# Performance work log

Hardware: AMD Instinct MI355X
Metric: run time of the kernel (lower is better)

Reference implementation:

```python
import jax, jax.numpy as jnp
import numpy as np

B, N, D_MODEL, H, DK, DV = 8, 512, 512, 8, 64, 64
MAX_DIST = 512
NUM_REL = 2 * MAX_DIST - 1  # 1023


def setup_inputs() -> dict:
    key = jax.random.key(0)
    ks = jax.random.split(key, 12)
    s = 0.02
    return {
        "X": jax.random.normal(ks[0], (B, N, D_MODEL), jnp.float32),
        "Wq": jax.random.normal(ks[1], (D_MODEL, H * DK), jnp.float32) * s,
        "bq": jnp.zeros((H * DK,), jnp.float32),
        "Wk": jax.random.normal(ks[2], (D_MODEL, H * DK), jnp.float32) * s,
        "bk": jnp.zeros((H * DK,), jnp.float32),
        "Wv": jax.random.normal(ks[3], (D_MODEL, H * DV), jnp.float32) * s,
        "bv": jnp.zeros((H * DV,), jnp.float32),
        "Wo": jax.random.normal(ks[4], (H * DV, D_MODEL), jnp.float32) * s,
        "bo": jnp.zeros((D_MODEL,), jnp.float32),
        "P_k": jax.random.normal(ks[5], (NUM_REL, H), jnp.float32),
        "P_v": jax.random.normal(ks[6], (NUM_REL, H, DV), jnp.float32),
    }


def reference(X, Wq, bq, Wk, bk, Wv, bv, Wo, bo, P_k, P_v):
    b, n, d = X.shape
    scale = 1.0 / jnp.sqrt(jnp.float32(DK))
    # projections -> [b, h, n, d]
    Q = (X @ Wq + bq).reshape(b, n, H, DK).transpose(0, 2, 1, 3)
    K = (X @ Wk + bk).reshape(b, n, H, DK).transpose(0, 2, 1, 3)
    V = (X @ Wv + bv).reshape(b, n, H, DV).transpose(0, 2, 1, 3)
    # relative index: rel[i, j] = zero_offset + (j - i)
    zero_offset = NUM_REL // 2
    rel = zero_offset + (jnp.arange(n)[None, :] - jnp.arange(n)[:, None])  # [n, n]
    A_k = P_k[rel]  # [n, n, h]
    scores = (jnp.einsum("bhid,bhjd->bhij", Q, K) + A_k.transpose(2, 0, 1)[None]) * scale
    attn = jax.nn.softmax(scores, axis=-1)  # [b, h, n, n]
    # standard value mixing + relative value mixing (einsum avoids the
    # explicit [b,h,n,n,dv] broadcast the torch code materializes; same math)
    A_v = P_v[rel]  # [n, n, h, dv]
    out = jnp.einsum("bhij,bhjd->bhid", attn, V) + jnp.einsum("bhij,ijhd->bhid", attn, A_v)
    out = out.transpose(0, 2, 1, 3).reshape(b, n, H * DV)
    return out @ Wo + bo
```

## Files before the change

### kernel.cpp

```cpp
#include <hip/hip_runtime.h>
#include <math.h>

#define Bc 8
#define Nseq 512
#define DM 512
#define Hh 8
#define NUMREL 1023
#define ZOFF 511
#define STR 552

typedef short bf16x8 __attribute__((ext_vector_type(8)));
typedef float f32x4 __attribute__((ext_vector_type(4)));

__device__ __forceinline__ unsigned short f2bf(float f) {
  unsigned u = __builtin_bit_cast(unsigned, f);
  u += 0x7fff + ((u >> 16) & 1);
  return (unsigned short)(u >> 16);
}
__device__ __forceinline__ float bf2f(unsigned short h) {
  unsigned u = ((unsigned)h) << 16;
  return __builtin_bit_cast(float, u);
}

typedef __attribute__((address_space(3))) unsigned int as3_uint;
typedef __attribute__((address_space(1))) const unsigned int as1_uint;
__device__ __forceinline__ void gl_lds16(const void* g, void* l) {
  __builtin_amdgcn_global_load_lds((as1_uint*)g, (as3_uint*)l, 16, 0, 0);
}

__global__ __launch_bounds__(256) void prep_all(
    const float* __restrict__ X, const float* __restrict__ Wq,
    const float* __restrict__ Wk, const float* __restrict__ Wv,
    const float* __restrict__ Wo, const float* __restrict__ Pk,
    const float* __restrict__ Pv,
    unsigned short* __restrict__ XbF, unsigned short* __restrict__ WqF,
    unsigned short* __restrict__ WkF, unsigned short* __restrict__ WvF,
    unsigned short* __restrict__ WoFh, unsigned short* __restrict__ WoFl,
    float* __restrict__ Pkt, unsigned short* __restrict__ PvF2) {
  __shared__ float tbuf[5120];
  const int bid = blockIdx.x;
  const int tid = threadIdx.x;

  if (bid < 1024) {
    const int w = tid >> 6, lane = tid & 63;
    const int r = bid * 4 + w;
    const float* src = X + (size_t)r * DM + lane * 8;
    float4 a = *(const float4*)src;
    float4 b = *(const float4*)(src + 4);
    ushort4 o0, o1;
    o0.x = f2bf(a.x); o0.y = f2bf(a.y); o0.z = f2bf(a.z); o0.w = f2bf(a.w);
    o1.x = f2bf(b.x); o1.y = f2bf(b.y); o1.z = f2bf(b.z); o1.w = f2bf(b.w);
    const int mc = r >> 4, kf = lane >> 2, l = (lane & 3) * 16 + (r & 15);
    size_t flat = (((size_t)mc * 16 + kf) * 64 + l) * 8;
    *(ushort4*)(XbF + flat) = o0;
    *(ushort4*)(XbF + flat + 4) = o1;
  } else if (bid < 2304) {
    const int idx = bid - 1024;
    const int z = idx >> 8, r256 = idx & 255;
    const int bx = r256 & 15, by = r256 >> 4;
    const float* src = z == 0 ? Wq : z == 1 ? Wk : z == 2 ? Wv : Wo;
    unsigned short* dst = z == 0 ? WqF : z == 1 ? WkF : z == 2 ? WvF : z == 3 ? WoFh : WoFl;
    const int k0 = by * 32, n0 = bx * 32;
#pragma unroll
    for (int u = 0; u < 4; ++u) {
      int i2 = u * 256 + tid, r = i2 >> 5, c = i2 & 31;
      tbuf[r * 33 + c] = src[(size_t)(k0 + r) * DM + n0 + c];
    }
    __syncthreads();
    const int ncl = tid >> 7, l = (tid >> 1) & 63, eh = tid & 1;
    const int nl = ncl * 16 + (l & 15);
    const int klb = (l >> 4) * 8 + eh * 4;
    ushort4 o;
    {
      float v0 = tbuf[(klb + 0) * 33 + nl], v1 = tbuf[(klb + 1) * 33 + nl];
      float v2 = tbuf[(klb + 2) * 33 + nl], v3 = tbuf[(klb + 3) * 33 + nl];
      unsigned short h0 = f2bf(v0), h1 = f2bf(v1), h2 = f2bf(v2), h3 = f2bf(v3);
      if (z == 4) {
        h0 = f2bf(v0 - bf2f(h0)); h1 = f2bf(v1 - bf2f(h1));
        h2 = f2bf(v2 - bf2f(h2)); h3 = f2bf(v3 - bf2f(h3));
      }
      o.x = h0; o.y = h1; o.z = h2; o.w = h3;
    }
    size_t flat = (((size_t)((n0 >> 4) + ncl) * 16 + (k0 >> 5)) * 64 + l) * 8 + eh * 4;
    *(ushort4*)(dst + flat) = o;
  } else if (bid < 2344) {
    const int idx = bid - 2304;
    const int gx = idx % 5, h = idx / 5;
    const int g = gx * 256 + tid;
    if (g < 1040)
      Pkt[(size_t)h * 1040 + g] = (g < NUMREL) ? Pk[(size_t)g * Hh + h] : 0.f;
  } else {
    const int idx = bid - 2344;
    const int gx = idx & 15, h = idx >> 4;
    const int g0 = gx * 64;
#pragma unroll
    for (int u = 0; u < 20; ++u) {
      int i2 = u * 256 + tid, r = i2 >> 6, c = i2 & 63;
      int g = g0 + r;
      tbuf[r * 64 + c] = (g < NUMREL) ? Pv[(size_t)g * 512 + h * 64 + c] : 0.f;
    }
    __syncthreads();
#pragma unroll
    for (int av = 0; av < 2; ++av)
#pragma unroll
      for (int gtl = 0; gtl < 2; ++gtl) {
        int gt = (g0 >> 5) + gtl;
#pragma unroll
        for (int dt = 0; dt < 4; ++dt) {
          size_t base = ((((size_t)av * Hh + h) * 4 + dt) * 32 + gt) * 512;
          int i2 = tid * 2;
          int l = i2 >> 3, e = i2 & 7;
          int gr = av * 16 + gtl * 32 + (l >> 4) * 8 + e;
          int dcol = dt * 16 + (l & 15);
          ushort2 o;
          o.x = f2bf(tbuf[gr * 64 + dcol]);
          o.y = f2bf(tbuf[(gr + 1) * 64 + dcol]);
          *(ushort2*)(PvF2 + base + i2) = o;
        }
      }
  }
}

__global__ __launch_bounds__(256, 2) void gemm_qkv(const unsigned short* __restrict__ XbF,
                                                   const unsigned short* __restrict__ WqF,
                                                   const unsigned short* __restrict__ WkF,
                                                   const unsigned short* __restrict__ WvF,
                                                   const float* __restrict__ bq,
                                                   const float* __restrict__ bk,
                                                   const float* __restrict__ bv,
                                                   unsigned short* __restrict__ Qb,
                                                   unsigned short* __restrict__ KF,
                                                   unsigned short* __restrict__ VF) {
  const int flat = blockIdx.x;
  const int xcd = flat & 7, g = flat >> 3;
  const int by = xcd * 8 + (g & 7), bx = g >> 3;
  const int bm = by * 64, bn = bx * 64;
  const int mc0 = bm >> 4, nc0 = bn >> 4;
  const int tid = threadIdx.x, w = tid >> 6, lane = tid & 63;
  const int lo = lane & 15, quad = lane >> 4;
  const int mh = (w >> 1) * 2, nh = (w & 1) * 2;

  __shared__ __align__(16) unsigned short stg[2][32 * 512];

  const unsigned short* srcArr = w == 0 ? XbF : w == 1 ? WqF : w == 2 ? WkF : WvF;
  const int rowbase = (w == 0) ? mc0 : nc0;

#define STAGE(buf, ks)                                                             \
  do {                                                                             \
    _Pragma("unroll") for (int t = 0; t < 8; ++t) {                                \
      gl_lds16(srcArr +                                                            \
                   (((size_t)(rowbase + (t >> 1)) * 16 + 2 * (ks) + (t & 1)) * 512) + \
                   lane * 8,                                                       \
               &stg[buf][(w * 8 + t) * 512]);                                      \
    }                                                                              \
  } while (0)

  f32x4 acc[3][2][2] = {};
  STAGE(0, 0);
  int cur = 0;
#pragma unroll
  for (int ks = 0; ks < 8; ++ks) {
    __syncthreads();
    if (ks < 7) STAGE(cur ^ 1, ks + 1);
#pragma unroll
    for (int kf = 0; kf < 2; ++kf) {
      bf16x8 af[2], bq_[2], bk_[2], bv_[2];
#pragma unroll
      for (int i = 0; i < 2; ++i)
        af[i] = *(const bf16x8*)(&stg[cur][((mh + i) * 2 + kf) * 512 + lane * 8]);
#pragma unroll
      for (int j = 0; j < 2; ++j) {
        bq_[j] = *(const bf16x8*)(&stg[cur][(8 + (nh + j) * 2 + kf) * 512 + lane * 8]);
        bk_[j] = *(const bf16x8*)(&stg[cur][(16 + (nh + j) * 2 + kf) * 512 + lane * 8]);
        bv_[j] = *(const bf16x8*)(&stg[cur][(24 + (nh + j) * 2 + kf) * 512 + lane * 8]);
      }
#pragma unroll
      for (int i = 0; i < 2; ++i)
#pragma unroll
        for (int j = 0; j < 2; ++j) {
          acc[0][i][j] = __builtin_amdgcn_mfma_f32_16x16x32_bf16(af[i], bq_[j], acc[0][i][j], 0, 0, 0);
          acc[1][i][j] = __builtin_amdgcn_mfma_f32_16x16x32_bf16(af[i], bk_[j], acc[1][i][j], 0, 0, 0);
          acc[2][i][j] = __builtin_amdgcn_mfma_f32_16x16x32_bf16(af[i], bv_[j], acc[2][i][j], 0, 0, 0);
        }
    }
    cur ^= 1;
  }
#undef STAGE

  const int mt = (w >> 1) * 32, nt = (w & 1) * 32;
#pragma unroll
  for (int z = 0; z < 3; ++z) {
    const float* bias = z == 0 ? bq : z == 1 ? bk : bv;
#pragma unroll
    for (int i = 0; i < 2; ++i)
#pragma unroll
      for (int j = 0; j < 2; ++j) {
        int col = bn + nt + j * 16 + lo;
        int h = col >> 6, d = col & 63;
        float bb = bias[col];
#pragma unroll
        for (int r = 0; r < 4; ++r) {
          int row = bm + mt + i * 16 + quad * 4 + r;
          int b = row >> 9, is = row & 511;
          int bh = b * Hh + h;
          unsigned short val = f2bf(acc[z][i][j][r] + bb);
          if (z == 0) {
            Qb[((size_t)bh * Nseq + is) * 64 + d] = val;
          } else if (z == 1) {
            int jt = is >> 4, kf2 = d >> 5, l = ((d >> 3) & 3) * 16 + (is & 15), e = d & 7;
            KF[(((size_t)bh * 32 + jt) * 2 + kf2) * 512 + l * 8 + e] = val;
          } else {
            int dt = d >> 4, ks = is >> 5, l = ((is >> 3) & 3) * 16 + (d & 15), e = is & 7;
            VF[(((size_t)bh * 4 + dt) * 16 + ks) * 512 + l * 8 + e] = val;
          }
        }
      }
  }
}

__global__ __launch_bounds__(256, 3) void attn_fused(
    const unsigned short* __restrict__ Qb,
    const unsigned short* __restrict__ KF,
    const unsigned short* __restrict__ VF,
    const float* __restrict__ Pkt,
    const unsigned short* __restrict__ PvF2,
    unsigned short* __restrict__ AwFh,
    unsigned short* __restrict__ AwFl) {
  const int flat = blockIdx.x;
  const int h = flat & 7;
  const int grp = flat >> 3;
  const int b = grp >> 4;
  const int p = grp & 15;
  const int itA = (p >> 1) * 4 + (p & 1);
  const int i0A = itA * 16;
  const int bh = b * Hh + h;
  const int tid = threadIdx.x, w = tid >> 6, lane = tid & 63;
  const int lo = lane & 15, quad = lane >> 4;

  __shared__ __align__(16) unsigned short stg[2][4096];
  __shared__ __align__(16) unsigned short pstA[16 * STR];
  __shared__ __align__(16) unsigned short pstB[16 * STR];
  __shared__ float pk_lds[560];

  const int TB = 464 - i0A;

  int4 z4; z4.x = z4.y = z4.z = z4.w = 0;
  for (int c = tid; c < 16 * STR / 8; c += 256) {
    ((int4*)pstA)[c] = z4;
    ((int4*)pstB)[c] = z4;
  }
  for (int c = tid; c < 140; c += 256)
    *(float4*)(pk_lds + c * 4) = *(const float4*)(Pkt + (size_t)h * 1040 + TB + c * 4);

  const unsigned short* qA = Qb + ((size_t)bh * Nseq + i0A + lo) * 64;
  const unsigned short* qB = Qb + ((size_t)bh * Nseq + i0A + 32 + lo) * 64;
  bf16x8 qa0 = *(const bf16x8*)(qA + quad * 8);
  bf16x8 qa1 = *(const bf16x8*)(qA + 32 + quad * 8);
  bf16x8 qb0 = *(const bf16x8*)(qB + quad * 8);
  bf16x8 qb1 = *(const bf16x8*)(qB + 32 + quad * 8);

  const unsigned short* KFb = KF + (size_t)bh * 64 * 512;
  const unsigned short* VFb = VF + ((size_t)bh * 4 + w) * 16 * 512;
  const int aP = (TB >> 4) & 1, gtB = TB >> 5;
  const unsigned short* PFb = PvF2 + ((((size_t)aP * Hh + h) * 4 + w) * 32 + gtB) * 512;

#define KSTAGE(g, buf)                                                     \
  do {                                                                     \
    _Pragma("unroll") for (int c = 0; c < 2; ++c)                          \
        gl_lds16(KFb + ((size_t)(w * 8 + (g)) * 2 + c) * 512 + lane * 8,   \
                 &stg[buf][(w * 2 + c) * 512]);                            \
  } while (0)
#define VSTAGE(g, buf)                                                     \
  do {                                                                     \
    _Pragma("unroll") for (int c = 0; c < 2; ++c)                          \
        gl_lds16(VFb + ((size_t)(2 * (g) + c)) * 512 + lane * 8,           \
                 &stg[buf][(w * 2 + c) * 512]);                            \
  } while (0)
#define PSTAGE(g, buf)                                                     \
  do {                                                                     \
    _Pragma("unroll") for (int c = 0; c < 2; ++c)                          \
        gl_lds16(PFb + ((size_t)(2 * (g) + c)) * 512 + lane * 8,           \
                 &stg[buf][(w * 2 + c) * 512]);                            \
  } while (0)

  KSTAGE(0, 0);
  __syncthreads();

  float svA[8][4], svB[8][4];
  float mA[4] = {-1e30f, -1e30f, -1e30f, -1e30f};
  float mB[4] = {-1e30f, -1e30f, -1e30f, -1e30f};
#pragma unroll
  for (int g = 0; g < 8; ++g) {
    bf16x8 k0 = *(const bf16x8*)(&stg[g & 1][(w * 2 + 0) * 512 + lane * 8]);
    bf16x8 k1 = *(const bf16x8*)(&stg[g & 1][(w * 2 + 1) * 512 + lane * 8]);
    if (g < 7) KSTAGE(g + 1, (g + 1) & 1);
    f32x4 cA = {0.f, 0.f, 0.f, 0.f};
    f32x4 cB = {0.f, 0.f, 0.f, 0.f};
    cA = __builtin_amdgcn_mfma_f32_16x16x32_bf16(qa0, k0, cA, 0, 0, 0);
    cA = __builtin_amdgcn_mfma_f32_16x16x32_bf16(qa1, k1, cA, 0, 0, 0);
    cB = __builtin_amdgcn_mfma_f32_16x16x32_bf16(qb0, k0, cB, 0, 0, 0);
    cB = __builtin_amdgcn_mfma_f32_16x16x32_bf16(qb1, k1, cB, 0, 0, 0);
    int j = w * 128 + g * 16 + lo;
#pragma unroll
    for (int r = 0; r < 4; ++r) {
      int rl = quad * 4 + r;
      int idx = j - rl + 15;
      float vA = (cA[r] + pk_lds[idx + 32]) * 0.125f;
      float vB = (cB[r] + pk_lds[idx]) * 0.125f;
      svA[g][r] = vA; svB[g][r] = vB;
      mA[r] = fmaxf(mA[r], vA);
      mB[r] = fmaxf(mB[r], vB);
    }
    __syncthreads();
  }

  float* redm = (float*)&stg[1][0];
  float* redl = (float*)&stg[1][256];
#pragma unroll
  for (int m = 1; m <= 8; m <<= 1)
#pragma unroll
    for (int r = 0; r < 4; ++r) {
      mA[r] = fmaxf(mA[r], __shfl_xor(mA[r], m));
      mB[r] = fmaxf(mB[r], __shfl_xor(mB[r], m));
    }
  if (lo == 0)
#pragma unroll
    for (int r = 0; r < 4; ++r) {
      redm[(0 * 4 + w) * 16 + quad * 4 + r] = mA[r];
      redm[(1 * 4 + w) * 16 + quad * 4 + r] = mB[r];
    }
  __syncthreads();
  float mfA[4], mfB[4];
#pragma unroll
  for (int r = 0; r < 4; ++r) {
    int rl = quad * 4 + r;
    mfA[r] = fmaxf(fmaxf(redm[rl], redm[16 + rl]), fmaxf(redm[32 + rl], redm[48 + rl]));
    mfB[r] = fmaxf(fmaxf(redm[64 + rl], redm[80 + rl]), fmaxf(redm[96 + rl], redm[112 + rl]));
  }
  float lA[4] = {0.f, 0.f, 0.f, 0.f}, lB[4] = {0.f, 0.f, 0.f, 0.f};
#pragma unroll
  for (int s = 0; s < 8; ++s)
#pragma unroll
    for (int r = 0; r < 4; ++r) {
      float eA = __expf(svA[s][r] - mfA[r]);
      float eB = __expf(svB[s][r] - mfB[r]);
      svA[s][r] = eA; svB[s][r] = eB;
      lA[r] += eA; lB[r] += eB;
    }
#pragma unroll
  for (int m = 1; m <= 8; m <<= 1)
#pragma unroll
    for (int r = 0; r < 4; ++r) {
      lA[r] += __shfl_xor(lA[r], m);
      lB[r] += __shfl_xor(lB[r], m);
    }
  if (lo == 0)
#pragma unroll
    for (int r = 0; r < 4; ++r) {
      redl[(0 * 4 + w) * 16 + quad * 4 + r] = lA[r];
      redl[(1 * 4 + w) * 16 + quad * 4 + r] = lB[r];
    }
  __syncthreads();
#pragma unroll
  for (int r = 0; r < 4; ++r) {
    int rl = quad * 4 + r;
    float liA = 1.f / (redl[rl] + redl[16 + rl] + redl[32 + rl] + redl[48 + rl]);
    float liB = 1.f / (redl[64 + rl] + redl[80 + rl] + redl[96 + rl] + redl[112 + rl]);
#pragma unroll
    for (int s = 0; s < 8; ++s) {
      int j = w * 128 + s * 16 + lo;
      pstA[rl * STR + 16 + j] = f2bf(svA[s][r] * liA);
      pstB[rl * STR + 16 + j] = f2bf(svB[s][r] * liB);
    }
  }
  VSTAGE(0, 0);
  __syncthreads();

  f32x4 oA = {0.f, 0.f, 0.f, 0.f};
  f32x4 oB = {0.f, 0.f, 0.f, 0.f};
#pragma unroll
  for (int g = 0; g < 8; ++g) {
    bf16x8 v0 = *(const bf16x8*)(&stg[g & 1][(w * 2 + 0) * 512 + lane * 8]);
    bf16x8 v1 = *(const bf16x8*)(&stg[g & 1][(w * 2 + 1) * 512 + lane * 8]);
    if (g < 7) VSTAGE(g + 1, (g + 1) & 1);
    else PSTAGE(0, 0);
#pragma unroll
    for (int c = 0; c < 2; ++c) {
      int ks = 2 * g + c;
      bf16x8 vv = c ? v1 : v0;
      bf16x8 pA = *(const bf16x8*)(&pstA[lo * STR + 16 + ks * 32 + quad * 8]);
      bf16x8 pB = *(const bf16x8*)(&pstB[lo * STR + 16 + ks * 32 + quad * 8]);
      oA = __builtin_amdgcn_mfma_f32_16x16x32_bf16(pA, vv, oA, 0, 0, 0);
      oB = __builtin_amdgcn_mfma_f32_16x16x32_bf16(pB, vv, oB, 0, 0, 0);
    }
    __syncthreads();
  }

#pragma unroll
  for (int g = 0; g < 9; ++g) {
    bf16x8 p0 = *(const bf16x8*)(&stg[g & 1][(w * 2 + 0) * 512 + lane * 8]);
    bf16x8 p1 = *(const bf16x8*)(&stg[g & 1][(w * 2 + 1) * 512 + lane * 8]);
    if (g < 8) PSTAGE(g + 1, (g + 1) & 1);
#pragma unroll
    for (int c = 0; c < 2; ++c) {
      int cg = 2 * g + c;
      bf16x8 pvf = c ? p1 : p0;
      if (cg < 17) {
        union { bf16x8 v; unsigned short s8[8]; } pa;
        if (cg == 16 && quad >= 2) {
#pragma unroll
          for (int e = 0; e < 8; ++e) pa.s8[e] = 0;
        } else {
          int base = lo * STR + cg * 32 + quad * 8 + lo + 1;
#pragma unroll
          for (int e = 0; e < 8; ++e) pa.s8[e] = pstB[base + e];
        }
        oB = __builtin_amdgcn_mfma_f32_16x16x32_bf16(pa.v, pvf, oB, 0, 0, 0);
      }
      if (cg >= 1) {
        int ksA = cg - 1;
        union { bf16x8 v; unsigned short s8[8]; } pa;
        if (ksA == 16 && quad >= 2) {
#pragma unroll
          for (int e = 0; e < 8; ++e) pa.s8[e] = 0;
        } else {
          int base = lo * STR + ksA * 32 + quad * 8 + lo + 1;
#pragma unroll
          for (int e = 0; e < 8; ++e) pa.s8[e] = pstA[base + e];
        }
        oA = __builtin_amdgcn_mfma_f32_16x16x32_bf16(pa.v, pvf, oA, 0, 0, 0);
      }
    }
    __syncthreads();
  }

  const int kf = h * 2 + (w >> 1);
  const int lhi = ((w & 1) * 2 + (lo >> 3)) * 16;
#pragma unroll
  for (int t = 0; t < 2; ++t) {
    f32x4 o = t ? oB : oA;
    int mc = b * 32 + itA + t * 2;
#pragma unroll
    for (int r = 0; r < 4; ++r) {
      float ov = o[r];
      unsigned short hi = f2bf(ov);
      unsigned short lov = f2bf(ov - bf2f(hi));
      size_t fl = (((size_t)mc * 16 + kf) * 64 + lhi + quad * 4 + r) * 8 + (lo & 7);
      AwFh[fl] = hi;
      AwFl[fl] = lov;
    }
  }
#undef KSTAGE
#undef VSTAGE
#undef PSTAGE
}

__global__ __launch_bounds__(256, 2) void gemm_final(const unsigned short* __restrict__ AhF,
                                                     const unsigned short* __restrict__ AlF,
                                                     const unsigned short* __restrict__ BhF,
                                                     const unsigned short* __restrict__ BlF,
                                                     const float* __restrict__ bo,
                                                     float* __restrict__ out) {
  const int flat = blockIdx.x;
  const int xcd = flat & 7, g = flat >> 3;
  const int by = xcd * 8 + (g & 7), bx = g >> 3;
  const int bm = by * 64, bn = bx * 64;
  const int mc0 = bm >> 4, nc0 = bn >> 4;
  const int tid = threadIdx.x, w = tid >> 6, lane = tid & 63;
  const int lo = lane & 15, quad = lane >> 4;
  const int mh = (w >> 1) * 2, nh = (w & 1) * 2;

  __shared__ __align__(16) unsigned short stg[2][32 * 512];

  const unsigned short* srcArr = w == 0 ? AhF : w == 1 ? AlF : w == 2 ? BhF : BlF;
  const int rowbase = (w < 2) ? mc0 : nc0;

#define STAGE2(buf, ks)                                                            \
  do {                                                                             \
    _Pragma("unroll") for (int t = 0; t < 8; ++t) {                                \
      gl_lds16(srcArr +                                                            \
                   (((size_t)(rowbase + (t >> 1)) * 16 + 2 * (ks) + (t & 1)) * 512) + \
                   lane * 8,                                                       \
               &stg[buf][(w * 8 + t) * 512]);                                      \
    }                                                                              \
  } while (0)

  f32x4 acc[2][2] = {};
  STAGE2(0, 0);
  int cur = 0;
#pragma unroll
  for (int ks = 0; ks < 8; ++ks) {
    __syncthreads();
    if (ks < 7) STAGE2(cur ^ 1, ks + 1);
#pragma unroll
    for (int kf = 0; kf < 2; ++kf) {
      bf16x8 ah[2], al[2], bh[2], bl[2];
#pragma unroll
      for (int i = 0; i < 2; ++i) {
        ah[i] = *(const bf16x8*)(&stg[cur][((mh + i) * 2 + kf) * 512 + lane * 8]);
        al[i] = *(const bf16x8*)(&stg[cur][(8 + (mh + i) * 2 + kf) * 512 + lane * 8]);
      }
#pragma unroll
      for (int j = 0; j < 2; ++j) {
        bh[j] = *(const bf16x8*)(&stg[cur][(16 + (nh + j) * 2 + kf) * 512 + lane * 8]);
        bl[j] = *(const bf16x8*)(&stg[cur][(24 + (nh + j) * 2 + kf) * 512 + lane * 8]);
      }
#pragma unroll
      for (int i = 0; i < 2; ++i)
#pragma unroll
        for (int j = 0; j < 2; ++j) {
          acc[i][j] = __builtin_amdgcn_mfma_f32_16x16x32_bf16(ah[i], bh[j], acc[i][j], 0, 0, 0);
          acc[i][j] = __builtin_amdgcn_mfma_f32_16x16x32_bf16(ah[i], bl[j], acc[i][j], 0, 0, 0);
          acc[i][j] = __builtin_amdgcn_mfma_f32_16x16x32_bf16(al[i], bh[j], acc[i][j], 0, 0, 0);
        }
    }
    cur ^= 1;
  }
#undef STAGE2

  const int mt = (w >> 1) * 32, nt = (w & 1) * 32;
#pragma unroll
  for (int i = 0; i < 2; ++i)
#pragma unroll
    for (int j = 0; j < 2; ++j) {
      int col = bn + nt + j * 16 + lo;
      float bb = bo[col];
#pragma unroll
      for (int r = 0; r < 4; ++r) {
        int row = bm + mt + i * 16 + quad * 4 + r;
        out[(size_t)row * DM + col] = acc[i][j][r] + bb;
      }
    }
}

extern "C" void kernel_launch(void* const* d_in, const int* in_sizes, int n_in,
                              void* d_out, int out_size, void* d_ws, size_t ws_size,
                              hipStream_t stream) {
  const float* X  = (const float*)d_in[0];
  const float* Wq = (const float*)d_in[1];
  const float* bq = (const float*)d_in[2];
  const float* Wk = (const float*)d_in[3];
  const float* bk = (const float*)d_in[4];
  const float* Wv = (const float*)d_in[5];
  const float* bv = (const float*)d_in[6];
  const float* Wo = (const float*)d_in[7];
  const float* bo = (const float*)d_in[8];
  const float* Pk = (const float*)d_in[9];
  const float* Pv = (const float*)d_in[10];
  float* out = (float*)d_out;

  char* p = (char*)d_ws;
  const size_t szX    = (size_t)Bc * Nseq * DM * 2;
  const size_t szW    = (size_t)DM * DM * 2;
  const size_t szPkt  = (size_t)Hh * 1040 * 4;
  const size_t szPvF2 = (size_t)2 * Hh * 4 * 32 * 512 * 2;
  const size_t szQKV  = (size_t)Bc * Hh * Nseq * 64 * 2;
  unsigned short* XbF  = (unsigned short*)p; p += szX;
  unsigned short* WqF  = (unsigned short*)p; p += szW;
  unsigned short* WkF  = (unsigned short*)p; p += szW;
  unsigned short* WvF  = (unsigned short*)p; p += szW;
  unsigned short* WoFh = (unsigned short*)p; p += szW;
  unsigned short* WoFl = (unsigned short*)p; p += szW;
  float*          Pkt  = (float*)p;          p += (szPkt + 255) & ~(size_t)255;
  unsigned short* PvF2 = (unsigned short*)p; p += szPvF2;
  unsigned short* Qb   = (unsigned short*)p; p += szQKV;
  unsigned short* KF   = (unsigned short*)p; p += szQKV;
  unsigned short* VF   = (unsigned short*)p; p += szQKV;
  unsigned short* AwFh = (unsigned short*)p; p += szX;
  unsigned short* AwFl = (unsigned short*)p; p += szX;

  dim3 blk(256);
  prep_all<<<dim3(2472), blk, 0, stream>>>(X, Wq, Wk, Wv, Wo, Pk, Pv,
                                           XbF, WqF, WkF, WvF, WoFh, WoFl, Pkt, PvF2);
  gemm_qkv<<<dim3(512), blk, 0, stream>>>(XbF, WqF, WkF, WvF, bq, bk, bv, Qb, KF, VF);
  attn_fused<<<dim3(1024), blk, 0, stream>>>(Qb, KF, VF, Pkt, PvF2, AwFh, AwFl);
  gemm_final<<<dim3(512), blk, 0, stream>>>(AwFh, AwFl, WoFh, WoFl, bo, out);
}
```

Measured before the change: 147.2 us.

## Switch bf16 pipeline to fp16 and drop split-precision output projection

Replaces bf16 conversions and MFMA calls with fp16 throughout, relying on fp16's extra mantissa bits to drop the hi/lo split for Wo and the attention output. This removes one weight-prep slice, halves the staged data and cuts MFMA count threefold in the final GEMM. Softmax normalization is deferred: unnormalized exponentials are written to LDS as fp16 and scaled at the end, with the value and relative-position accumulators kept separate. Risks fp16 range overflow or precision loss on the unnormalized probabilities and weights.

```diff
diff --git a/kernel.cpp b/kernel.cpp
--- a/kernel.cpp
+++ b/kernel.cpp
@@ -9,17 +9,12 @@
 #define ZOFF 511
 #define STR 552
 
-typedef short bf16x8 __attribute__((ext_vector_type(8)));
+typedef _Float16 half8 __attribute__((ext_vector_type(8)));
 typedef float f32x4 __attribute__((ext_vector_type(4)));
 
-__device__ __forceinline__ unsigned short f2bf(float f) {
-  unsigned u = __builtin_bit_cast(unsigned, f);
-  u += 0x7fff + ((u >> 16) & 1);
-  return (unsigned short)(u >> 16);
-}
-__device__ __forceinline__ float bf2f(unsigned short h) {
-  unsigned u = ((unsigned)h) << 16;
-  return __builtin_bit_cast(float, u);
+__device__ __forceinline__ unsigned short f2h(float f) {
+  _Float16 h = (_Float16)f;
+  return __builtin_bit_cast(unsigned short, h);
 }
 
 typedef __attribute__((address_space(3))) unsigned int as3_uint;
@@ -35,7 +30,7 @@
     const float* __restrict__ Pv,
     unsigned short* __restrict__ XbF, unsigned short* __restrict__ WqF,
     unsigned short* __restrict__ WkF, unsigned short* __restrict__ WvF,
-    unsigned short* __restrict__ WoFh, unsigned short* __restrict__ WoFl,
+    unsigned short* __restrict__ WoF,
     float* __restrict__ Pkt, unsigned short* __restrict__ PvF2) {
   __shared__ float tbuf[5120];
   const int bid = blockIdx.x;
@@ -48,18 +43,18 @@
     float4 a = *(const float4*)src;
     float4 b = *(const float4*)(src + 4);
     ushort4 o0, o1;
-    o0.x = f2bf(a.x); o0.y = f2bf(a.y); o0.z = f2bf(a.z); o0.w = f2bf(a.w);
-    o1.x = f2bf(b.x); o1.y = f2bf(b.y); o1.z = f2bf(b.z); o1.w = f2bf(b.w);
+    o0.x = f2h(a.x); o0.y = f2h(a.y); o0.z = f2h(a.z); o0.w = f2h(a.w);
+    o1.x = f2h(b.x); o1.y = f2h(b.y); o1.z = f2h(b.z); o1.w = f2h(b.w);
     const int mc = r >> 4, kf = lane >> 2, l = (lane & 3) * 16 + (r & 15);
     size_t flat = (((size_t)mc * 16 + kf) * 64 + l) * 8;
     *(ushort4*)(XbF + flat) = o0;
     *(ushort4*)(XbF + flat + 4) = o1;
-  } else if (bid < 2304) {
+  } else if (bid < 2048) {
     const int idx = bid - 1024;
     const int z = idx >> 8, r256 = idx & 255;
     const int bx = r256 & 15, by = r256 >> 4;
     const float* src = z == 0 ? Wq : z == 1 ? Wk : z == 2 ? Wv : Wo;
-    unsigned short* dst = z == 0 ? WqF : z == 1 ? WkF : z == 2 ? WvF : z == 3 ? WoFh : WoFl;
+    unsigned short* dst = z == 0 ? WqF : z == 1 ? WkF : z == 2 ? WvF : WoF;
     const int k0 = by * 32, n0 = bx * 32;
 #pragma unroll
     for (int u = 0; u < 4; ++u) {
@@ -71,26 +66,20 @@
     const int nl = ncl * 16 + (l & 15);
     const int klb = (l >> 4) * 8 + eh * 4;
     ushort4 o;
-    {
-      float v0 = tbuf[(klb + 0) * 33 + nl], v1 = tbuf[(klb + 1) * 33 + nl];
-      float v2 = tbuf[(klb + 2) * 33 + nl], v3 = tbuf[(klb + 3) * 33 + nl];
-      unsigned short h0 = f2bf(v0), h1 = f2bf(v1), h2 = f2bf(v2), h3 = f2bf(v3);
-      if (z == 4) {
-        h0 = f2bf(v0 - bf2f(h0)); h1 = f2bf(v1 - bf2f(h1));
-        h2 = f2bf(v2 - bf2f(h2)); h3 = f2bf(v3 - bf2f(h3));
-      }
-      o.x = h0; o.y = h1; o.z = h2; o.w = h3;
-    }
+    o.x = f2h(tbuf[(klb + 0) * 33 + nl]);
+    o.y = f2h(tbuf[(klb + 1) * 33 + nl]);
+    o.z = f2h(tbuf[(klb + 2) * 33 + nl]);
+    o.w = f2h(tbuf[(klb + 3) * 33 + nl]);
     size_t flat = (((size_t)((n0 >> 4) + ncl) * 16 + (k0 >> 5)) * 64 + l) * 8 + eh * 4;
     *(ushort4*)(dst + flat) = o;
-  } else if (bid < 2344) {
-    const int idx = bid - 2304;
+  } else if (bid < 2088) {
+    const int idx = bid - 2048;
     const int gx = idx % 5, h = idx / 5;
     const int g = gx * 256 + tid;
     if (g < 1040)
       Pkt[(size_t)h * 1040 + g] = (g < NUMREL) ? Pk[(size_t)g * Hh + h] : 0.f;
   } else {
-    const int idx = bid - 2344;
+    const int idx = bid - 2088;
     const int gx = idx & 15, h = idx >> 4;
     const int g0 = gx * 64;
 #pragma unroll
@@ -113,8 +102,8 @@
           int gr = av * 16 + gtl * 32 + (l >> 4) * 8 + e;
           int dcol = dt * 16 + (l & 15);
           ushort2 o;
-          o.x = f2bf(tbuf[gr * 64 + dcol]);
-          o.y = f2bf(tbuf[(gr + 1) * 64 + dcol]);
+          o.x = f2h(tbuf[gr * 64 + dcol]);
+          o.y = f2h(tbuf[(gr + 1) * 64 + dcol]);
           *(ushort2*)(PvF2 + base + i2) = o;
         }
       }
@@ -164,23 +153,23 @@
     if (ks < 7) STAGE(cur ^ 1, ks + 1);
 #pragma unroll
     for (int kf = 0; kf < 2; ++kf) {
-      bf16x8 af[2], bq_[2], bk_[2], bv_[2];
+      half8 af[2], bq_[2], bk_[2], bv_[2];
 #pragma unroll
       for (int i = 0; i < 2; ++i)
-        af[i] = *(const bf16x8*)(&stg[cur][((mh + i) * 2 + kf) * 512 + lane * 8]);
+        af[i] = *(const half8*)(&stg[cur][((mh + i) * 2 + kf) * 512 + lane * 8]);
 #pragma unroll
       for (int j = 0; j < 2; ++j) {
-        bq_[j] = *(const bf16x8*)(&stg[cur][(8 + (nh + j) * 2 + kf) * 512 + lane * 8]);
-        bk_[j] = *(const bf16x8*)(&stg[cur][(16 + (nh + j) * 2 + kf) * 512 + lane * 8]);
-        bv_[j] = *(const bf16x8*)(&stg[cur][(24 + (nh + j) * 2 + kf) * 512 + lane * 8]);
+        bq_[j] = *(const half8*)(&stg[cur][(8 + (nh + j) * 2 + kf) * 512 + lane * 8]);
+        bk_[j] = *(const half8*)(&stg[cur][(16 + (nh + j) * 2 + kf) * 512 + lane * 8]);
+        bv_[j] = *(const half8*)(&stg[cur][(24 + (nh + j) * 2 + kf) * 512 + lane * 8]);
       }
 #pragma unroll
       for (int i = 0; i < 2; ++i)
 #pragma unroll
         for (int j = 0; j < 2; ++j) {
-          acc[0][i][j] = __builtin_amdgcn_mfma_f32_16x16x32_bf16(af[i], bq_[j], acc[0][i][j], 0, 0, 0);
-          acc[1][i][j] = __builtin_amdgcn_mfma_f32_16x16x32_bf16(af[i], bk_[j], acc[1][i][j], 0, 0, 0);
-          acc[2][i][j] = __builtin_amdgcn_mfma_f32_16x16x32_bf16(af[i], bv_[j], acc[2][i][j], 0, 0, 0);
+          acc[0][i][j] = __builtin_amdgcn_mfma_f32_16x16x32_f16(af[i], bq_[j], acc[0][i][j], 0, 0, 0);
+          acc[1][i][j] = __builtin_amdgcn_mfma_f32_16x16x32_f16(af[i], bk_[j], acc[1][i][j], 0, 0, 0);
+          acc[2][i][j] = __builtin_amdgcn_mfma_f32_16x16x32_f16(af[i], bv_[j], acc[2][i][j], 0, 0, 0);
         }
     }
     cur ^= 1;
@@ -203,7 +192,7 @@
           int row = bm + mt + i * 16 + quad * 4 + r;
           int b = row >> 9, is = row & 511;
           int bh = b * Hh + h;
-          unsigned short val = f2bf(acc[z][i][j][r] + bb);
+          unsigned short val = f2h(acc[z][i][j][r] + bb);
           if (z == 0) {
             Qb[((size_t)bh * Nseq + is) * 64 + d] = val;
           } else if (z == 1) {
@@ -224,8 +213,7 @@
     const unsigned short* __restrict__ VF,
     const float* __restrict__ Pkt,
     const unsigned short* __restrict__ PvF2,
-    unsigned short* __restrict__ AwFh,
-    unsigned short* __restrict__ AwFl) {
+    unsigned short* __restrict__ AwF) {
   const int flat = blockIdx.x;
   const int h = flat & 7;
   const int grp = flat >> 3;
@@ -254,10 +242,10 @@
 
   const unsigned short* qA = Qb + ((size_t)bh * Nseq + i0A + lo) * 64;
   const unsigned short* qB = Qb + ((size_t)bh * Nseq + i0A + 32 + lo) * 64;
-  bf16x8 qa0 = *(const bf16x8*)(qA + quad * 8);
-  bf16x8 qa1 = *(const bf16x8*)(qA + 32 + quad * 8);
-  bf16x8 qb0 = *(const bf16x8*)(qB + quad * 8);
-  bf16x8 qb1 = *(const bf16x8*)(qB + 32 + quad * 8);
+  half8 qa0 = *(const half8*)(qA + quad * 8);
+  half8 qa1 = *(const half8*)(qA + 32 + quad * 8);
+  half8 qb0 = *(const half8*)(qB + quad * 8);
+  half8 qb1 = *(const half8*)(qB + 32 + quad * 8);
 
   const unsigned short* KFb = KF + (size_t)bh * 64 * 512;
   const unsigned short* VFb = VF + ((size_t)bh * 4 + w) * 16 * 512;
@@ -291,15 +279,15 @@
   float mB[4] = {-1e30f, -1e30f, -1e30f, -1e30f};
 #pragma unroll
   for (int g = 0; g < 8; ++g) {
-    bf16x8 k0 = *(const bf16x8*)(&stg[g & 1][(w * 2 + 0) * 512 + lane * 8]);
-    bf16x8 k1 = *(const bf16x8*)(&stg[g & 1][(w * 2 + 1) * 512 + lane * 8]);
+    half8 k0 = *(const half8*)(&stg[g & 1][(w * 2 + 0) * 512 + lane * 8]);
+    half8 k1 = *(const half8*)(&stg[g & 1][(w * 2 + 1) * 512 + lane * 8]);
     if (g < 7) KSTAGE(g + 1, (g + 1) & 1);
     f32x4 cA = {0.f, 0.f, 0.f, 0.f};
     f32x4 cB = {0.f, 0.f, 0.f, 0.f};
-    cA = __builtin_amdgcn_mfma_f32_16x16x32_bf16(qa0, k0, cA, 0, 0, 0);
-    cA = __builtin_amdgcn_mfma_f32_16x16x32_bf16(qa1, k1, cA, 0, 0, 0);
-    cB = __builtin_amdgcn_mfma_f32_16x16x32_bf16(qb0, k0, cB, 0, 0, 0);
-    cB = __builtin_amdgcn_mfma_f32_16x16x32_bf16(qb1, k1, cB, 0, 0, 0);
+    cA = __builtin_amdgcn_mfma_f32_16x16x32_f16(qa0, k0, cA, 0, 0, 0);
+    cA = __builtin_amdgcn_mfma_f32_16x16x32_f16(qa1, k1, cA, 0, 0, 0);
+    cB = __builtin_amdgcn_mfma_f32_16x16x32_f16(qb0, k0, cB, 0, 0, 0);
+    cB = __builtin_amdgcn_mfma_f32_16x16x32_f16(qb1, k1, cB, 0, 0, 0);
     int j = w * 128 + g * 16 + lo;
 #pragma unroll
     for (int r = 0; r < 4; ++r) {
@@ -361,52 +349,53 @@
       redl[(1 * 4 + w) * 16 + quad * 4 + r] = lB[r];
     }
   __syncthreads();
+  float liA[4], liB[4];
 #pragma unroll
   for (int r = 0; r < 4; ++r) {
     int rl = quad * 4 + r;
-    float liA = 1.f / (redl[rl] + redl[16 + rl] + redl[32 + rl] + redl[48 + rl]);
-    float liB = 1.f / (redl[64 + rl] + redl[80 + rl] + redl[96 + rl] + redl[112 + rl]);
+    liA[r] = 1.f / (redl[rl] + redl[16 + rl] + redl[32 + rl] + redl[48 + rl]);
+    liB[r] = 1.f / (redl[64 + rl] + redl[80 + rl] + redl[96 + rl] + redl[112 + rl]);
 #pragma unroll
     for (int s = 0; s < 8; ++s) {
       int j = w * 128 + s * 16 + lo;
-      pstA[rl * STR + 16 + j] = f2bf(svA[s][r] * liA);
-      pstB[rl * STR + 16 + j] = f2bf(svB[s][r] * liB);
+      pstA[rl * STR + 16 + j] = f2h(svA[s][r]);
+      pstB[rl * STR + 16 + j] = f2h(svB[s][r]);
     }
   }
   VSTAGE(0, 0);
   __syncthreads();
 
-  f32x4 oA = {0.f, 0.f, 0.f, 0.f};
-  f32x4 oB = {0.f, 0.f, 0.f, 0.f};
+  f32x4 oVA = {0.f, 0.f, 0.f, 0.f}, oVB = {0.f, 0.f, 0.f, 0.f};
 #pragma unroll
   for (int g = 0; g < 8; ++g) {
-    bf16x8 v0 = *(const bf16x8*)(&stg[g & 1][(w * 2 + 0) * 512 + lane * 8]);
-    bf16x8 v1 = *(const bf16x8*)(&stg[g & 1][(w * 2 + 1) * 512 + lane * 8]);
+    half8 v0 = *(const half8*)(&stg[g & 1][(w * 2 + 0) * 512 + lane * 8]);
+    half8 v1 = *(const half8*)(&stg[g & 1][(w * 2 + 1) * 512 + lane * 8]);
     if (g < 7) VSTAGE(g + 1, (g + 1) & 1);
     else PSTAGE(0, 0);
 #pragma unroll
     for (int c = 0; c < 2; ++c) {
       int ks = 2 * g + c;
-      bf16x8 vv = c ? v1 : v0;
-      bf16x8 pA = *(const bf16x8*)(&pstA[lo * STR + 16 + ks * 32 + quad * 8]);
-      bf16x8 pB = *(const bf16x8*)(&pstB[lo * STR + 16 + ks * 32 + quad * 8]);
-      oA = __builtin_amdgcn_mfma_f32_16x16x32_bf16(pA, vv, oA, 0, 0, 0);
-      oB = __builtin_amdgcn_mfma_f32_16x16x32_bf16(pB, vv, oB, 0, 0, 0);
-    }
-    __syncthreads();
-  }
-
+      half8 vv = c ? v1 : v0;
+      half8 pA = *(const half8*)(&pstA[lo * STR + 16 + ks * 32 + quad * 8]);
+      half8 pB = *(const half8*)(&pstB[lo * STR + 16 + ks * 32 + quad * 8]);
+      oVA = __builtin_amdgcn_mfma_f32_16x16x32_f16(pA, vv, oVA, 0, 0, 0);
+      oVB = __builtin_amdgcn_mfma_f32_16x16x32_f16(pB, vv, oVB, 0, 0, 0);
+    }
+    __syncthreads();
+  }
+
+  f32x4 oPA = {0.f, 0.f, 0.f, 0.f}, oPB = {0.f, 0.f, 0.f, 0.f};
 #pragma unroll
   for (int g = 0; g < 9; ++g) {
-    bf16x8 p0 = *(const bf16x8*)(&stg[g & 1][(w * 2 + 0) * 512 + lane * 8]);
-    bf16x8 p1 = *(const bf16x8*)(&stg[g & 1][(w * 2 + 1) * 512 + lane * 8]);
+    half8 p0 = *(const half8*)(&stg[g & 1][(w * 2 + 0) * 512 + lane * 8]);
+    half8 p1 = *(const half8*)(&stg[g & 1][(w * 2 + 1) * 512 + lane * 8]);
     if (g < 8) PSTAGE(g + 1, (g + 1) & 1);
 #pragma unroll
     for (int c = 0; c < 2; ++c) {
       int cg = 2 * g + c;
-      bf16x8 pvf = c ? p1 : p0;
+      half8 pvf = c ? p1 : p0;
       if (cg < 17) {
-        union { bf16x8 v; unsigned short s8[8]; } pa;
+        union { half8 v; unsigned short s8[8]; } pa;
         if (cg == 16 && quad >= 2) {
 #pragma unroll
           for (int e = 0; e < 8; ++e) pa.s8[e] = 0;
@@ -415,11 +404,11 @@
 #pragma unroll
           for (int e = 0; e < 8; ++e) pa.s8[e] = pstB[base + e];
         }
-        oB = __builtin_amdgcn_mfma_f32_16x16x32_bf16(pa.v, pvf, oB, 0, 0, 0);
+        oPB = __builtin_amdgcn_mfma_f32_16x16x32_f16(pa.v, pvf, oPB, 0, 0, 0);
       }
       if (cg >= 1) {
         int ksA = cg - 1;
-        union { bf16x8 v; unsigned short s8[8]; } pa;
+        union { half8 v; unsigned short s8[8]; } pa;
         if (ksA == 16 && quad >= 2) {
 #pragma unroll
           for (int e = 0; e < 8; ++e) pa.s8[e] = 0;
@@ -428,7 +417,7 @@
 #pragma unroll
           for (int e = 0; e < 8; ++e) pa.s8[e] = pstA[base + e];
         }
-        oA = __builtin_amdgcn_mfma_f32_16x16x32_bf16(pa.v, pvf, oA, 0, 0, 0);
+        oPA = __builtin_amdgcn_mfma_f32_16x16x32_f16(pa.v, pvf, oPA, 0, 0, 0);
       }
     }
     __syncthreads();
@@ -438,16 +427,12 @@
   const int lhi = ((w & 1) * 2 + (lo >> 3)) * 16;
 #pragma unroll
   for (int t = 0; t < 2; ++t) {
-    f32x4 o = t ? oB : oA;
     int mc = b * 32 + itA + t * 2;
 #pragma unroll
     for (int r = 0; r < 4; ++r) {
-      float ov = o[r];
-      unsigned short hi = f2bf(ov);
-      unsigned short lov = f2bf(ov - bf2f(hi));
+      float ov = t ? (oVB[r] + oPB[r]) * liB[r] : (oVA[r] + oPA[r]) * liA[r];
       size_t fl = (((size_t)mc * 16 + kf) * 64 + lhi + quad * 4 + r) * 8 + (lo & 7);
-      AwFh[fl] = hi;
-      AwFl[fl] = lov;
+      AwF[fl] = f2h(ov);
     }
   }
 #undef KSTAGE
@@ -455,10 +440,8 @@
 #undef PSTAGE
 }
 
-__global__ __launch_bounds__(256, 2) void gemm_final(const unsigned short* __restrict__ AhF,
-                                                     const unsigned short* __restrict__ AlF,
-                                                     const unsigned short* __restrict__ BhF,
-                                                     const unsigned short* __restrict__ BlF,
+__global__ __launch_bounds__(256, 2) void gemm_final(const unsigned short* __restrict__ AF,
+                                                     const unsigned short* __restrict__ BF,
                                                      const float* __restrict__ bo,
                                                      float* __restrict__ out) {
   const int flat = blockIdx.x;
@@ -470,18 +453,18 @@
   const int lo = lane & 15, quad = lane >> 4;
   const int mh = (w >> 1) * 2, nh = (w & 1) * 2;
 
-  __shared__ __align__(16) unsigned short stg[2][32 * 512];
-
-  const unsigned short* srcArr = w == 0 ? AhF : w == 1 ? AlF : w == 2 ? BhF : BlF;
-  const int rowbase = (w < 2) ? mc0 : nc0;
+  __shared__ __align__(16) unsigned short stg[2][16 * 512];
+
+  const unsigned short* srcArr = (w < 2) ? AF : BF;
+  const int rowbase = ((w < 2) ? mc0 : nc0) + (w & 1) * 2;
 
 #define STAGE2(buf, ks)                                                            \
   do {                                                                             \
-    _Pragma("unroll") for (int t = 0; t < 8; ++t) {                                \
+    _Pragma("unroll") for (int t = 0; t < 4; ++t) {                                \
       gl_lds16(srcArr +                                                            \
                    (((size_t)(rowbase + (t >> 1)) * 16 + 2 * (ks) + (t & 1)) * 512) + \
                    lane * 8,                                                       \
-               &stg[buf][(w * 8 + t) * 512]);                                      \
+               &stg[buf][(w * 4 + t) * 512]);                                      \
     }                                                                              \
   } while (0)
 
@@ -494,25 +477,18 @@
     if (ks < 7) STAGE2(cur ^ 1, ks + 1);
 #pragma unroll
     for (int kf = 0; kf < 2; ++kf) {
-      bf16x8 ah[2], al[2], bh[2], bl[2];
-#pragma unroll
-      for (int i = 0; i < 2; ++i) {
-        ah[i] = *(const bf16x8*)(&stg[cur][((mh + i) * 2 + kf) * 512 + lane * 8]);
-        al[i] = *(const bf16x8*)(&stg[cur][(8 + (mh + i) * 2 + kf) * 512 + lane * 8]);
-      }
-#pragma unroll
-      for (int j = 0; j < 2; ++j) {
-        bh[j] = *(const bf16x8*)(&stg[cur][(16 + (nh + j) * 2 + kf) * 512 + lane * 8]);
-        bl[j] = *(const bf16x8*)(&stg[cur][(24 + (nh + j) * 2 + kf) * 512 + lane * 8]);
-      }
+      half8 af[2], bf[2];
 #pragma unroll
       for (int i = 0; i < 2; ++i)
-#pragma unroll
-        for (int j = 0; j < 2; ++j) {
-          acc[i][j] = __builtin_amdgcn_mfma_f32_16x16x32_bf16(ah[i], bh[j], acc[i][j], 0, 0, 0);
-          acc[i][j] = __builtin_amdgcn_mfma_f32_16x16x32_bf16(ah[i], bl[j], acc[i][j], 0, 0, 0);
-          acc[i][j] = __builtin_amdgcn_mfma_f32_16x16x32_bf16(al[i], bh[j], acc[i][j], 0, 0, 0);
-        }
+        af[i] = *(const half8*)(&stg[cur][((mh + i) * 2 + kf) * 512 + lane * 8]);
+#pragma unroll
+      for (int j = 0; j < 2; ++j)
+        bf[j] = *(const half8*)(&stg[cur][(8 + (nh + j) * 2 + kf) * 512 + lane * 8]);
+#pragma unroll
+      for (int i = 0; i < 2; ++i)
+#pragma unroll
+        for (int j = 0; j < 2; ++j)
+          acc[i][j] = __builtin_amdgcn_mfma_f32_16x16x32_f16(af[i], bf[j], acc[i][j], 0, 0, 0);
     }
     cur ^= 1;
   }
@@ -555,24 +531,22 @@
   const size_t szPkt  = (size_t)Hh * 1040 * 4;
   const size_t szPvF2 = (size_t)2 * Hh * 4 * 32 * 512 * 2;
   const size_t szQKV  = (size_t)Bc * Hh * Nseq * 64 * 2;
-  unsigned short* XbF  = (unsigned short*)p; p += szX;
-  unsigned short* WqF  = (unsigned short*)p; p += szW;
-  unsigned short* WkF  = (unsigned short*)p; p += szW;
-  unsigned short* WvF  = (unsigned short*)p; p += szW;
-  unsigned short* WoFh = (unsigned short*)p; p += szW;
-  unsigned short* WoFl = (unsigned short*)p; p += szW;
-  float*          Pkt  = (float*)p;          p += (szPkt + 255) & ~(size_t)255;
+  unsigned short* XbF = (unsigned short*)p; p += szX;
+  unsigned short* WqF = (unsigned short*)p; p += szW;
+  unsigned short* WkF = (unsigned short*)p; p += szW;
+  unsigned short* WvF = (unsigned short*)p; p += szW;
+  unsigned short* WoF = (unsigned short*)p; p += szW;
+  float*          Pkt = (float*)p;          p += (szPkt + 255) & ~(size_t)255;
   unsigned short* PvF2 = (unsigned short*)p; p += szPvF2;
-  unsigned short* Qb   = (unsigned short*)p; p += szQKV;
-  unsigned short* KF   = (unsigned short*)p; p += szQKV;
-  unsigned short* VF   = (unsigned short*)p; p += szQKV;
-  unsigned short* AwFh = (unsigned short*)p; p += szX;
-  unsigned short* AwFl = (unsigned short*)p; p += szX;
+  unsigned short* Qb  = (unsigned short*)p; p += szQKV;
+  unsigned short* KF  = (unsigned short*)p; p += szQKV;
+  unsigned short* VF  = (unsigned short*)p; p += szQKV;
+  unsigned short* AwF = (unsigned short*)p; p += szX;
 
   dim3 blk(256);
-  prep_all<<<dim3(2472), blk, 0, stream>>>(X, Wq, Wk, Wv, Wo, Pk, Pv,
-                                           XbF, WqF, WkF, WvF, WoFh, WoFl, Pkt, PvF2);
+  prep_all<<<dim3(2216), blk, 0, stream>>>(X, Wq, Wk, Wv, Wo, Pk, Pv,
+                                           XbF, WqF, WkF, WvF, WoF, Pkt, PvF2);
   gemm_qkv<<<dim3(512), blk, 0, stream>>>(XbF, WqF, WkF, WvF, bq, bk, bv, Qb, KF, VF);
-  attn_fused<<<dim3(1024), blk, 0, stream>>>(Qb, KF, VF, Pkt, PvF2, AwFh, AwFl);
-  gemm_final<<<dim3(512), blk, 0, stream>>>(AwFh, AwFl, WoFh, WoFl, bo, out);
-}
+  attn_fused<<<dim3(1024), blk, 0, stream>>>(Qb, KF, VF, Pkt, PvF2, AwF);
+  gemm_final<<<dim3(512), blk, 0, stream>>>(AwF, WoF, bo, out);
+}
```

Result: faster. 143.3 us (-2.6%).
